# Performance work log

Hardware: AMD Instinct MI355X
Metric: run time of the kernel (lower is better)

The kernel has to match this reference:

```python
import jax, jax.numpy as jnp
import numpy as np

N, E, D, H = 100000, 800000, 128, 4
DK = D // H
SCALE = 1.0 / np.sqrt(D)  # keep logits tame with random weights
EPS = 1e-5


def _layernorm(x, g, b):
    mu = jnp.mean(x, axis=-1, keepdims=True)
    var = jnp.mean(jnp.square(x - mu), axis=-1, keepdims=True)
    return (x - mu) * jax.lax.rsqrt(var + EPS) * g + b


def setup_inputs() -> dict:
    key = jax.random.key(0)
    ks = jax.random.split(key, 14)
    inp = {
        'h': jax.random.normal(ks[0], (N, D), jnp.float32),
        'e_ij': jax.random.normal(ks[1], (E, D), jnp.float32),
        'W1': jax.random.normal(ks[2], (D, D), jnp.float32) * SCALE,
        'W2': jax.random.normal(ks[3], (D, D), jnp.float32) * SCALE,
        'W3': jax.random.normal(ks[4], (D, D), jnp.float32) * SCALE,
        'W4': jax.random.normal(ks[5], (D, D), jnp.float32) * SCALE,
        'W5': jax.random.normal(ks[6], (D, D), jnp.float32) * SCALE,
        'W6': jax.random.normal(ks[7], (D, D), jnp.float32) * SCALE,
        'ln_gamma': jnp.ones((D,), jnp.float32),
        'ln_beta': jnp.zeros((D,), jnp.float32),
        'mlp_w1': jax.random.normal(ks[8], (D, 2 * D), jnp.float32) * SCALE,
        'mlp_w2': jax.random.normal(ks[9], (2 * D, D), jnp.float32) * (1.0 / np.sqrt(2 * D)),
        'src': jax.random.randint(ks[10], (E,), 0, N, jnp.int32),
        'dst': jax.random.randint(ks[11], (E,), 0, N, jnp.int32),
    }
    return inp


def reference(h, e_ij, W1, W2, W3, W4, W5, W6, ln_gamma, ln_beta, mlp_w1, mlp_w2, src, dst):
    u = (h @ W1).reshape(N, H, DK)      # src-side query
    v = (h @ W2).reshape(N, H, DK)      # dst-side
    x3 = (e_ij @ W3).reshape(E, H, DK)
    # m = v[dst] + x_ij ; attn = u[src] * m (elementwise per head/channel)
    m = v[dst] + x3                      # [E,H,DK]
    attn = (u[src] * m) / np.sqrt(DK)    # [E,H,DK]
    # edge_softmax: segment softmax over incoming edges of each dst node
    amax = jax.ops.segment_max(attn, dst, num_segments=N)   # [N,H,DK]
    ex = jnp.exp(attn - amax[dst])
    denom = jax.ops.segment_sum(ex, dst, num_segments=N)    # [N,H,DK]
    alpha = ex / denom[dst]
    k = (h @ W4).reshape(N, H, DK)
    x5 = (e_ij @ W5).reshape(E, H, DK)
    m2 = k[dst] + x5                     # [E,H,DK]
    agg = jax.ops.segment_sum(alpha * m2, dst, num_segments=N).reshape(N, D)
    h1 = h @ W6 + agg
    h1 = _layernorm(h1, ln_gamma, ln_beta)
    mlp_out = jax.nn.relu(h1 @ mlp_w1) @ mlp_w2
    h2 = _layernorm(h1 + mlp_out, ln_gamma, ln_beta)  # same LayerNorm params reused
    return h2
```

## Files before the change

### kernel.cpp

```cpp
#include <hip/hip_runtime.h>
#include <hip/hip_bf16.h>

#define N_NODES 100000
#define N_EDGES 800000

typedef __attribute__((ext_vector_type(8))) short short8v;
typedef __attribute__((ext_vector_type(4))) float f32x4;

__device__ __forceinline__ unsigned short f2bf(float f) {
    __hip_bfloat16 b = __float2bfloat16(f);
    return *(unsigned short*)&b;
}
__device__ __forceinline__ float bf2f(unsigned short u) {
    return __uint_as_float((unsigned)u << 16);
}
__device__ __forceinline__ unsigned pack2(float lo, float hi) {
    return (unsigned)f2bf(lo) | ((unsigned)f2bf(hi) << 16);
}

__device__ __forceinline__ void gload_lds16(const void* g, void* l) {
    __builtin_amdgcn_global_load_lds(
        (const __attribute__((address_space(1))) unsigned int*)g,
        (__attribute__((address_space(3))) unsigned int*)l,
        16, 0, 0);
}

__device__ __forceinline__ int xcd_swizzle(int orig, int q, int r) {
    int xcd = orig & 7, loc = orig >> 3;
    return (xcd < r ? xcd * (q + 1) : r * (q + 1) + (xcd - r) * q) + loc;
}

__global__ __launch_bounds__(256) void hist_dst(
    const int* __restrict__ dst, int* __restrict__ counts)
{
    int e = blockIdx.x * 256 + threadIdx.x;
    if (e < N_EDGES) atomicAdd(&counts[dst[e]], 1);
}

__global__ __launch_bounds__(256) void scan_p1(
    const int* __restrict__ in, int* __restrict__ partials, int n)
{
    __shared__ int ws[4];
    int t = threadIdx.x, lane = t & 63, wv = t >> 6;
    int base = blockIdx.x * 1024;
    int s = 0;
#pragma unroll
    for (int i = 0; i < 4; ++i) {
        int idx = base + i * 256 + t;
        s += (idx < n) ? in[idx] : 0;
    }
#pragma unroll
    for (int off = 1; off < 64; off <<= 1) s += __shfl_xor(s, off);
    if (lane == 0) ws[wv] = s;
    __syncthreads();
    if (t == 0) partials[blockIdx.x] = ws[0] + ws[1] + ws[2] + ws[3];
}

__global__ __launch_bounds__(64) void scan_p2(
    int* __restrict__ partials, int nb, int* __restrict__ total_out)
{
    int lane = threadIdx.x;
    int carry = 0;
    for (int base = 0; base < nb; base += 64) {
        int idx = base + lane;
        int v = (idx < nb) ? partials[idx] : 0;
        int s = v;
#pragma unroll
        for (int off = 1; off < 64; off <<= 1) {
            int w = __shfl_up(s, off);
            if (lane >= off) s += w;
        }
        if (idx < nb) partials[idx] = s - v + carry;
        carry += __shfl(s, 63);
    }
    if (lane == 0) *total_out = carry;
}

__global__ __launch_bounds__(256) void scan_p3(
    const int* __restrict__ in, int* __restrict__ out, int* __restrict__ cursor,
    const int* __restrict__ partials, int n)
{
    __shared__ int ws[4];
    __shared__ int wpre[4];
    __shared__ int s_tot;
    int t = threadIdx.x, lane = t & 63, wv = t >> 6;
    int base = blockIdx.x * 1024;
    int carry = partials[blockIdx.x];
    for (int sub = 0; sub < 4; ++sub) {
        int idx = base + sub * 256 + t;
        int v = (idx < n) ? in[idx] : 0;
        int s = v;
#pragma unroll
        for (int off = 1; off < 64; off <<= 1) {
            int w = __shfl_up(s, off);
            if (lane >= off) s += w;
        }
        if (lane == 63) ws[wv] = s;
        __syncthreads();
        if (t == 0) {
            int a = 0;
#pragma unroll
            for (int i = 0; i < 4; ++i) { wpre[i] = a; a += ws[i]; }
            s_tot = a;
        }
        __syncthreads();
        int excl = s - v + wpre[wv] + carry;
        if (idx < n) { out[idx] = excl; if (cursor) cursor[idx] = excl; }
        carry += s_tot;
        __syncthreads();
    }
}

__global__ __launch_bounds__(256) void scatter_edges(
    const int* __restrict__ dst, const int* __restrict__ src,
    int* __restrict__ cursor,
    int* __restrict__ edge_ord, int* __restrict__ src_ord,
    int* __restrict__ dst_ord)
{
    int e = blockIdx.x * 256 + threadIdx.x;
    if (e < N_EDGES) {
        int d = dst[e];
        int pos = atomicAdd(&cursor[d], 1);
        edge_ord[pos] = e;
        src_ord[pos] = src[e];
        dst_ord[pos] = d;
    }
}

__global__ __launch_bounds__(256) void calc_npieces(
    const int* __restrict__ offsets, int* __restrict__ npieces)
{
    int n = blockIdx.x * 256 + threadIdx.x;
    if (n < N_NODES) {
        int b = offsets[n], e = offsets[n + 1];
        npieces[n] = (e > b) ? (((e - 1) >> 6) - (b >> 6) + 1) : 0;
    }
}

__global__ __launch_bounds__(256) void prep_weights(
    const float* __restrict__ W1, const float* __restrict__ W2,
    const float* __restrict__ W3, const float* __restrict__ W4,
    const float* __restrict__ W5, const float* __restrict__ W6,
    const float* __restrict__ mw1, const float* __restrict__ mw2,
    unsigned short* __restrict__ w3t, unsigned short* __restrict__ w5t,
    unsigned short* __restrict__ wcatt,
    unsigned short* __restrict__ mw1t, unsigned short* __restrict__ mw2t)
{
    int bid = blockIdx.x;
    if (bid < 64) {
        int t = bid * 256 + threadIdx.x;
        int r = t >> 7, c = t & 127;
        w3t[c * 128 + r] = f2bf(W3[t]);
        w5t[c * 128 + r] = f2bf(W5[t]);
    } else if (bid < 320) {
        int t = (bid - 64) * 256 + threadIdx.x;
        int n = t >> 7, k = t & 127;
        const float* Wm = (n < 128) ? W1 : (n < 256) ? W2 : (n < 384) ? W4 : W6;
        wcatt[t] = f2bf(Wm[k * 128 + (n & 127)]);
    } else {
        int t = (bid - 320) * 256 + threadIdx.x;
        if (t < 32768) {
            int n = t >> 7, k = t & 127;
            mw1t[t] = f2bf(mw1[k * 256 + n]);
        } else {
            int s = t - 32768;
            int n = s >> 8, k = s & 255;
            mw2t[s] = f2bf(mw2[k * 128 + n]);
        }
    }
}

__global__ __launch_bounds__(256) void gemm_node(
    const float* __restrict__ A, const unsigned short* __restrict__ Bt,
    unsigned short* __restrict__ uvkb, float* __restrict__ hw6f)
{
    const int nwg = 1563 * 4;
    const int l = xcd_swizzle((int)blockIdx.x, nwg >> 3, nwg & 7);
    const int m0 = (l >> 2) * 64;
    const int n0 = (l & 3) * 128;

    const int t = threadIdx.x;
    const int lane = t & 63, wv = t >> 6;
    const int l15 = lane & 15, kg = lane >> 4;
    const int M = N_NODES, K = 128;

    int arow = m0 + wv * 16 + l15;
    int arow_c = arow < M ? arow : M - 1;
    const float* ap = A + (size_t)arow_c * K + kg * 8;

    f32x4 acc[8];
#pragma unroll
    for (int nt = 0; nt < 8; ++nt) acc[nt] = (f32x4){0.f, 0.f, 0.f, 0.f};

    for (int ko = 0; ko < K; ko += 32) {
        float4 f0 = *(const float4*)(ap + ko);
        float4 f1 = *(const float4*)(ap + ko + 4);
        short8v af;
        af[0] = (short)f2bf(f0.x); af[1] = (short)f2bf(f0.y);
        af[2] = (short)f2bf(f0.z); af[3] = (short)f2bf(f0.w);
        af[4] = (short)f2bf(f1.x); af[5] = (short)f2bf(f1.y);
        af[6] = (short)f2bf(f1.z); af[7] = (short)f2bf(f1.w);
#pragma unroll
        for (int nt = 0; nt < 8; ++nt) {
            short8v bf = *(const short8v*)(Bt + (size_t)(n0 + nt * 16 + l15) * K + ko + kg * 8);
            acc[nt] = __builtin_amdgcn_mfma_f32_16x16x32_bf16(af, bf, acc[nt], 0, 0, 0);
        }
    }
#pragma unroll
    for (int nt = 0; nt < 8; ++nt) {
#pragma unroll
        for (int r = 0; r < 4; ++r) {
            int row = m0 + wv * 16 + kg * 4 + r;
            if (row < M) {
                int col = n0 + nt * 16 + l15;
                float vfl = acc[nt][r];
                if (n0 < 384) uvkb[(size_t)row * 384 + col] = f2bf(vfl);
                else          hw6f[(size_t)row * 128 + col - 384] = vfl;
            }
        }
    }
}

__global__ __launch_bounds__(256) void gemm_bf16(
    const unsigned short* __restrict__ A, const unsigned short* __restrict__ Bt,
    int M, int K, int Nc,
    const float* __restrict__ res, float* __restrict__ Cf,
    unsigned short* __restrict__ Cb, int do_relu)
{
    const int t = threadIdx.x;
    const int lane = t & 63, wv = t >> 6;
    const int l15 = lane & 15, kg = lane >> 4;
    const int m0 = blockIdx.x * 64;
    const int n0 = blockIdx.y * 128;

    int arow = m0 + wv * 16 + l15;
    int arow_c = arow < M ? arow : M - 1;
    const unsigned short* ap = A + (size_t)arow_c * K + kg * 8;

    f32x4 acc[8];
#pragma unroll
    for (int nt = 0; nt < 8; ++nt) acc[nt] = (f32x4){0.f, 0.f, 0.f, 0.f};

    for (int ko = 0; ko < K; ko += 32) {
        short8v af = *(const short8v*)(ap + ko);
#pragma unroll
        for (int nt = 0; nt < 8; ++nt) {
            short8v bf = *(const short8v*)(Bt + (size_t)(n0 + nt * 16 + l15) * K + ko + kg * 8);
            acc[nt] = __builtin_amdgcn_mfma_f32_16x16x32_bf16(af, bf, acc[nt], 0, 0, 0);
        }
    }
#pragma unroll
    for (int nt = 0; nt < 8; ++nt) {
#pragma unroll
        for (int r = 0; r < 4; ++r) {
            int row = m0 + wv * 16 + kg * 4 + r;
            if (row < M) {
                int col = n0 + nt * 16 + l15;
                float vfl = acc[nt][r];
                if (res) vfl += res[(size_t)row * Nc + col];
                if (do_relu) vfl = fmaxf(vfl, 0.f);
                if (Cf) Cf[(size_t)row * Nc + col] = vfl;
                else    Cb[(size_t)row * Nc + col] = f2bf(vfl);
            }
        }
    }
}

__global__ __launch_bounds__(256) void gemm_bf16_ln(
    const unsigned short* __restrict__ A, const unsigned short* __restrict__ Bt,
    int M, int K, const float* __restrict__ res,
    const float* __restrict__ gamma, const float* __restrict__ beta,
    float* __restrict__ out)
{
    const int t = threadIdx.x;
    const int lane = t & 63, wv = t >> 6;
    const int l15 = lane & 15, kg = lane >> 4;
    const int m0 = blockIdx.x * 64;

    int arow = m0 + wv * 16 + l15;
    int arow_c = arow < M ? arow : M - 1;
    const unsigned short* ap = A + (size_t)arow_c * K + kg * 8;

    f32x4 acc[8];
#pragma unroll
    for (int nt = 0; nt < 8; ++nt) acc[nt] = (f32x4){0.f, 0.f, 0.f, 0.f};

    for (int ko = 0; ko < K; ko += 32) {
        short8v af = *(const short8v*)(ap + ko);
#pragma unroll
        for (int nt = 0; nt < 8; ++nt) {
            short8v bf = *(const short8v*)(Bt + (size_t)(nt * 16 + l15) * K + ko + kg * 8);
            acc[nt] = __builtin_amdgcn_mfma_f32_16x16x32_bf16(af, bf, acc[nt], 0, 0, 0);
        }
    }

    float gv[8], bv[8];
#pragma unroll
    for (int nt = 0; nt < 8; ++nt) {
        gv[nt] = gamma[nt * 16 + l15];
        bv[nt] = beta[nt * 16 + l15];
    }

#pragma unroll
    for (int r = 0; r < 4; ++r) {
        int row = m0 + wv * 16 + kg * 4 + r;
        int rc = row < M ? row : M - 1;
        float x[8];
        float s = 0.f;
#pragma unroll
        for (int nt = 0; nt < 8; ++nt) {
            x[nt] = acc[nt][r] + res[(size_t)rc * 128 + nt * 16 + l15];
            s += x[nt];
        }
#pragma unroll
        for (int off = 1; off < 16; off <<= 1) s += __shfl_xor(s, off);
        float mu = s * (1.f / 128.f);
        float ss = 0.f;
#pragma unroll
        for (int nt = 0; nt < 8; ++nt) {
            float d = x[nt] - mu;
            ss += d * d;
        }
#pragma unroll
        for (int off = 1; off < 16; off <<= 1) ss += __shfl_xor(ss, off);
        float rsv = rsqrtf(ss * (1.f / 128.f) + 1e-5f);
        if (row < M) {
#pragma unroll
            for (int nt = 0; nt < 8; ++nt)
                out[(size_t)row * 128 + nt * 16 + l15] =
                    (x[nt] - mu) * rsv * gv[nt] + bv[nt];
        }
    }
}

__global__ __launch_bounds__(256, 4) void edge_agg(
    const float* __restrict__ e_ij,
    const unsigned short* __restrict__ w3t, const unsigned short* __restrict__ w5t,
    const unsigned short* __restrict__ uvkb,
    const int* __restrict__ edge_ord, const int* __restrict__ src_ord,
    const int* __restrict__ dst_ord,
    const int* __restrict__ offsets, const int* __restrict__ ppos,
    float* __restrict__ dpart, float* __restrict__ apart)
{
    __shared__ __align__(16) float e_s[64 * 128];
    __shared__ int s_eid[64], s_src[64], s_dst[64];
    __shared__ int s_sb[64], s_se[64], s_pi[64];
    __shared__ int s_nseg;

    const int t  = threadIdx.x;
    const int lane = t & 63, wv = t >> 6;
    const int l15 = lane & 15, kg = lane >> 4;
    const int cb = wv * 32 + 2 * l15;
    const float inv = 0.17677669529663687f;

    const int nwg = N_EDGES / 64;
    const int bswz = xcd_swizzle((int)blockIdx.x, nwg >> 3, nwg & 7);
    const int e0 = bswz * 64;

    if (t < 64) {
        s_eid[t] = edge_ord[e0 + t];
        s_src[t] = src_ord[e0 + t];
        int d = dst_ord[e0 + t];
        s_dst[t] = d;
        int dprev = __shfl_up(d, 1);
        bool bnd = (t == 0) || (d != dprev);
        unsigned long long mask = __ballot(bnd);
        int sid = __popcll(mask & ((1ull << t) - 1ull));
        if (bnd) {
            s_sb[sid] = t;
            s_pi[sid] = ppos[d] + bswz - (offsets[d] >> 6);
            if (t > 0) s_se[sid - 1] = t;
        }
        if (t == 63) {
            int ns = __popcll(mask);
            s_se[ns - 1] = 64;
            s_nseg = ns;
        }
    }
    __syncthreads();

#pragma unroll
    for (int i = 0; i < 8; ++i) {
        int c = i * 256 + t;
        int row = c >> 5, j = c & 31;
        int js = j ^ (row & 7);
        const float* g = e_ij + (size_t)s_eid[row] * 128 + js * 4;
        void* l = (void*)((char*)(&e_s[0]) + (size_t)i * 4096 + (size_t)wv * 1024);
        gload_lds16(g, l);
    }
    __syncthreads();

    unsigned short* eb = (unsigned short*)&e_s[0];
    {
        const int crow = t >> 2, q = t & 3;
        float4 fr[8];
#pragma unroll
        for (int i = 0; i < 8; ++i) {
            int j = (q * 8 + i) ^ (crow & 7);
            fr[i] = *(const float4*)(&e_s[crow * 128 + j * 4]);
        }
        __syncthreads();
#pragma unroll
        for (int i = 0; i < 4; ++i) {
            short8v pk;
            pk[0] = (short)f2bf(fr[2 * i].x);     pk[1] = (short)f2bf(fr[2 * i].y);
            pk[2] = (short)f2bf(fr[2 * i].z);     pk[3] = (short)f2bf(fr[2 * i].w);
            pk[4] = (short)f2bf(fr[2 * i + 1].x); pk[5] = (short)f2bf(fr[2 * i + 1].y);
            pk[6] = (short)f2bf(fr[2 * i + 1].z); pk[7] = (short)f2bf(fr[2 * i + 1].w);
            int c = (q * 4 + i) ^ (crow & 15);
            *(short8v*)(eb + crow * 128 + c * 8) = pk;
        }
    }
    __syncthreads();

    const int nseg = __builtin_amdgcn_readfirstlane(s_nseg);

    f32x4 a3[4][2], a5[4][2];
#pragma unroll
    for (int m = 0; m < 4; ++m) {
        a3[m][0] = (f32x4){0.f, 0.f, 0.f, 0.f};
        a3[m][1] = (f32x4){0.f, 0.f, 0.f, 0.f};
        a5[m][0] = (f32x4){0.f, 0.f, 0.f, 0.f};
        a5[m][1] = (f32x4){0.f, 0.f, 0.f, 0.f};
    }
    {
        const unsigned short* b3p0 = w3t + (size_t)(cb + 0) * 128 + kg * 8;
        const unsigned short* b3p1 = w3t + (size_t)(cb + 1) * 128 + kg * 8;
        const unsigned short* b5p0 = w5t + (size_t)(cb + 0) * 128 + kg * 8;
        const unsigned short* b5p1 = w5t + (size_t)(cb + 1) * 128 + kg * 8;
#pragma unroll
        for (int kidx = 0; kidx < 4; ++kidx) {
            const int ko = kidx * 32;
            short8v b30 = *(const short8v*)(b3p0 + ko);
            short8v b31 = *(const short8v*)(b3p1 + ko);
            short8v b50 = *(const short8v*)(b5p0 + ko);
            short8v b51 = *(const short8v*)(b5p1 + ko);
#pragma unroll
            for (int m = 0; m < 4; ++m) {
                const int row = m * 16 + l15;
                short8v af = *(const short8v*)(eb + row * 128 + (((kidx << 2) | kg) ^ l15) * 8);
                a3[m][0] = __builtin_amdgcn_mfma_f32_16x16x32_bf16(af, b30, a3[m][0], 0, 0, 0);
                a3[m][1] = __builtin_amdgcn_mfma_f32_16x16x32_bf16(af, b31, a3[m][1], 0, 0, 0);
                a5[m][0] = __builtin_amdgcn_mfma_f32_16x16x32_bf16(af, b50, a5[m][0], 0, 0, 0);
                a5[m][1] = __builtin_amdgcn_mfma_f32_16x16x32_bf16(af, b51, a5[m][1], 0, 0, 0);
            }
        }
    }

#pragma unroll
    for (int m = 0; m < 4; ++m) {
#pragma unroll
        for (int r = 0; r < 4; ++r) {
            int le = m * 16 + kg * 4 + r;
            int d  = s_dst[le];
            int sv = s_src[le];
            unsigned upk = *(const unsigned*)&uvkb[(size_t)sv * 384 + cb];
            unsigned vpk = *(const unsigned*)&uvkb[(size_t)d * 384 + 128 + cb];
            float u0 = bf2f((unsigned short)(upk & 0xffffu));
            float u1 = bf2f((unsigned short)(upk >> 16));
            float v0 = bf2f((unsigned short)(vpk & 0xffffu));
            float v1 = bf2f((unsigned short)(vpk >> 16));
            float at0 = u0 * (v0 + a3[m][0][r]) * inv;
            float at1 = u1 * (v1 + a3[m][1][r]) * inv;
            float ex0 = __expf(fminf(at0, 80.f));
            float ex1 = __expf(fminf(at1, 80.f));
            a3[m][0][r] = ex0;
            a3[m][1][r] = ex1;
            a5[m][0][r] = ex0 * a5[m][0][r];
            a5[m][1][r] = ex1 * a5[m][1][r];
        }
    }

    for (int sg = 0; sg < nseg; ++sg) {
        const int b  = __builtin_amdgcn_readfirstlane(s_sb[sg]);
        const int e2 = __builtin_amdgcn_readfirstlane(s_se[sg]);
        const int pi = __builtin_amdgcn_readfirstlane(s_pi[sg]);
        float d0 = 0.f, d1 = 0.f, g0 = 0.f, g1 = 0.f;
#pragma unroll
        for (int m = 0; m < 4; ++m) {
            if (b < m * 16 + 16 && e2 > m * 16) {
#pragma unroll
                for (int r = 0; r < 4; ++r) {
                    int slot = m * 16 + kg * 4 + r;
                    bool in = (slot >= b) && (slot < e2);
                    d0 += in ? a3[m][0][r] : 0.f;
                    d1 += in ? a3[m][1][r] : 0.f;
                    g0 += in ? a5[m][0][r] : 0.f;
                    g1 += in ? a5[m][1][r] : 0.f;
                }
            }
        }
        d0 += __shfl_xor(d0, 16); d0 += __shfl_xor(d0, 32);
        d1 += __shfl_xor(d1, 16); d1 += __shfl_xor(d1, 32);
        g0 += __shfl_xor(g0, 16); g0 += __shfl_xor(g0, 32);
        g1 += __shfl_xor(g1, 16); g1 += __shfl_xor(g1, 32);
        if (kg == 0) {
            *(float2*)&dpart[(size_t)pi * 128 + cb] = make_float2(d0, d1);
            *(float2*)&apart[(size_t)pi * 128 + cb] = make_float2(g0, g1);
        }
    }
}

__global__ __launch_bounds__(256) void node_finalize(
    const float* __restrict__ hw6f, const unsigned short* __restrict__ uvkb,
    const float* __restrict__ dpart, const float* __restrict__ apart,
    const int* __restrict__ ppos,
    const float* __restrict__ gamma, const float* __restrict__ beta,
    float* __restrict__ h1, unsigned short* __restrict__ h1b)
{
    int n = blockIdx.x * 4 + (threadIdx.x >> 6);
    int lane = threadIdx.x & 63;
    int p0 = ppos[n], p1 = ppos[n + 1];
    float de0 = 0.f, de1 = 0.f, g0 = 0.f, g1 = 0.f;
    for (int j = p0; j < p1; ++j) {
        float2 dv = *(const float2*)&dpart[(size_t)j * 128 + lane * 2];
        float2 av = *(const float2*)&apart[(size_t)j * 128 + lane * 2];
        de0 += dv.x; de1 += dv.y;
        g0  += av.x; g1  += av.y;
    }
    unsigned kpk = *(const unsigned*)&uvkb[(size_t)n * 384 + 256 + lane * 2];
    float k0 = bf2f((unsigned short)(kpk & 0xffffu));
    float k1 = bf2f((unsigned short)(kpk >> 16));
    float2 hw = *(const float2*)&hw6f[(size_t)n * 128 + lane * 2];
    float x0 = hw.x + (de0 > 0.f ? k0 + g0 / de0 : 0.f);
    float x1 = hw.y + (de1 > 0.f ? k1 + g1 / de1 : 0.f);
    float s = x0 + x1;
#pragma unroll
    for (int off = 1; off < 64; off <<= 1) s += __shfl_xor(s, off);
    float mu = s * (1.f / 128.f);
    float d0 = x0 - mu, d1 = x1 - mu;
    float ss = d0 * d0 + d1 * d1;
#pragma unroll
    for (int off = 1; off < 64; off <<= 1) ss += __shfl_xor(ss, off);
    float rs = rsqrtf(ss * (1.f / 128.f) + 1e-5f);
    float2 g = *(const float2*)&gamma[lane * 2];
    float2 b = *(const float2*)&beta[lane * 2];
    float o0 = d0 * rs * g.x + b.x;
    float o1 = d1 * rs * g.y + b.y;
    size_t base = (size_t)n * 128 + lane * 2;
    *(float2*)&h1[base] = make_float2(o0, o1);
    *(unsigned*)&h1b[base] = pack2(o0, o1);
}

extern "C" void kernel_launch(void* const* d_in, const int* in_sizes, int n_in,
                              void* d_out, int out_size, void* d_ws, size_t ws_size,
                              hipStream_t stream)
{
    const float* h    = (const float*)d_in[0];
    const float* e_ij = (const float*)d_in[1];
    const float* W1   = (const float*)d_in[2];
    const float* W2   = (const float*)d_in[3];
    const float* W3   = (const float*)d_in[4];
    const float* W4   = (const float*)d_in[5];
    const float* W5   = (const float*)d_in[6];
    const float* W6   = (const float*)d_in[7];
    const float* ln_g = (const float*)d_in[8];
    const float* ln_b = (const float*)d_in[9];
    const float* mw1  = (const float*)d_in[10];
    const float* mw2  = (const float*)d_in[11];
    const int*   src  = (const int*)d_in[12];
    const int*   dst  = (const int*)d_in[13];
    float* out = (float*)d_out;

    float* ws = (float*)d_ws;
    float* hw6f  = ws;
    float* h1    = ws + 12800000;
    float* dpart = ws + 25600000;
    float* apart = ws + 40100000;
    unsigned short* uvkb    = (unsigned short*)(ws + 54600000);
    unsigned short* h1b     = (unsigned short*)(ws + 73800000);
    unsigned short* hiddenb = (unsigned short*)(ws + 80200000);
    unsigned short* w3t   = (unsigned short*)(ws + 93000000);
    unsigned short* w5t   = w3t + 16384;
    unsigned short* wcatt = w5t + 16384;
    unsigned short* mw1t  = wcatt + 65536;
    unsigned short* mw2t  = mw1t + 32768;
    int* ibase    = (int*)(ws + 93100000);
    int* counts   = ibase;
    int* offsets  = ibase + 100000;
    int* cursor   = ibase + 200001;
    int* npieces  = ibase + 300001;
    int* ppos     = ibase + 400001;
    int* partials = ibase + 500102;
    int* edge_ord = ibase + 500230;
    int* src_ord  = edge_ord + N_EDGES;
    int* dst_ord  = src_ord + N_EDGES;

    dim3 blk(256);
    hipMemsetAsync(counts, 0, N_NODES * sizeof(int), stream);

    hist_dst<<<N_EDGES / 256, blk, 0, stream>>>(dst, counts);
    scan_p1<<<98, blk, 0, stream>>>(counts, partials, N_NODES);
    scan_p2<<<1, 64, 0, stream>>>(partials, 98, offsets + N_NODES);
    scan_p3<<<98, blk, 0, stream>>>(counts, offsets, cursor, partials, N_NODES);
    scatter_edges<<<N_EDGES / 256, blk, 0, stream>>>(dst, src, cursor,
                                                     edge_ord, src_ord, dst_ord);
    calc_npieces<<<391, blk, 0, stream>>>(offsets, npieces);
    scan_p1<<<98, blk, 0, stream>>>(npieces, partials, N_NODES);
    scan_p2<<<1, 64, 0, stream>>>(partials, 98, ppos + N_NODES);
    scan_p3<<<98, blk, 0, stream>>>(npieces, ppos, (int*)nullptr, partials, N_NODES);

    prep_weights<<<576, blk, 0, stream>>>(W1, W2, W3, W4, W5, W6, mw1, mw2,
                                          w3t, w5t, wcatt, mw1t, mw2t);

    gemm_node<<<1563 * 4, blk, 0, stream>>>(h, wcatt, uvkb, hw6f);

    edge_agg<<<N_EDGES / 64, blk, 0, stream>>>(e_ij, w3t, w5t, uvkb,
                                               edge_ord, src_ord, dst_ord,
                                               offsets, ppos, dpart, apart);

    node_finalize<<<N_NODES / 4, blk, 0, stream>>>(hw6f, uvkb, dpart, apart, ppos,
                                                   ln_g, ln_b, h1, h1b);

    gemm_bf16<<<dim3(1563, 2), blk, 0, stream>>>(h1b, mw1t, N_NODES, 128, 256,
                                                 nullptr, nullptr, hiddenb, 1);
    gemm_bf16_ln<<<1563, blk, 0, stream>>>(hiddenb, mw2t, N_NODES, 256,
                                           h1, ln_g, ln_b, out);
}
```

Baseline: 636.9 us.

## Fuse node finalize, MLP GEMMs and final LayerNorm into one kernel

```diff
diff --git a/kernel.cpp b/kernel.cpp
--- a/kernel.cpp
+++ b/kernel.cpp
@@ -174,14 +174,11 @@
     const float* __restrict__ A, const unsigned short* __restrict__ Bt,
     unsigned short* __restrict__ uvkb, float* __restrict__ hw6f)
 {
-    const int nwg = 1563 * 4;
-    const int l = xcd_swizzle((int)blockIdx.x, nwg >> 3, nwg & 7);
-    const int m0 = (l >> 2) * 64;
-    const int n0 = (l & 3) * 128;
-
     const int t = threadIdx.x;
     const int lane = t & 63, wv = t >> 6;
     const int l15 = lane & 15, kg = lane >> 4;
+    const int m0 = blockIdx.x * 64;
+    const int n0 = blockIdx.y * 128;
     const int M = N_NODES, K = 128;
 
     int arow = m0 + wv * 16 + l15;
@@ -217,118 +214,6 @@
                 if (n0 < 384) uvkb[(size_t)row * 384 + col] = f2bf(vfl);
                 else          hw6f[(size_t)row * 128 + col - 384] = vfl;
             }
-        }
-    }
-}
-
-__global__ __launch_bounds__(256) void gemm_bf16(
-    const unsigned short* __restrict__ A, const unsigned short* __restrict__ Bt,
-    int M, int K, int Nc,
-    const float* __restrict__ res, float* __restrict__ Cf,
-    unsigned short* __restrict__ Cb, int do_relu)
-{
-    const int t = threadIdx.x;
-    const int lane = t & 63, wv = t >> 6;
-    const int l15 = lane & 15, kg = lane >> 4;
-    const int m0 = blockIdx.x * 64;
-    const int n0 = blockIdx.y * 128;
-
-    int arow = m0 + wv * 16 + l15;
-    int arow_c = arow < M ? arow : M - 1;
-    const unsigned short* ap = A + (size_t)arow_c * K + kg * 8;
-
-    f32x4 acc[8];
-#pragma unroll
-    for (int nt = 0; nt < 8; ++nt) acc[nt] = (f32x4){0.f, 0.f, 0.f, 0.f};
-
-    for (int ko = 0; ko < K; ko += 32) {
-        short8v af = *(const short8v*)(ap + ko);
-#pragma unroll
-        for (int nt = 0; nt < 8; ++nt) {
-            short8v bf = *(const short8v*)(Bt + (size_t)(n0 + nt * 16 + l15) * K + ko + kg * 8);
-            acc[nt] = __builtin_amdgcn_mfma_f32_16x16x32_bf16(af, bf, acc[nt], 0, 0, 0);
-        }
-    }
-#pragma unroll
-    for (int nt = 0; nt < 8; ++nt) {
-#pragma unroll
-        for (int r = 0; r < 4; ++r) {
-            int row = m0 + wv * 16 + kg * 4 + r;
-            if (row < M) {
-                int col = n0 + nt * 16 + l15;
-                float vfl = acc[nt][r];
-                if (res) vfl += res[(size_t)row * Nc + col];
-                if (do_relu) vfl = fmaxf(vfl, 0.f);
-                if (Cf) Cf[(size_t)row * Nc + col] = vfl;
-                else    Cb[(size_t)row * Nc + col] = f2bf(vfl);
-            }
-        }
-    }
-}
-
-__global__ __launch_bounds__(256) void gemm_bf16_ln(
-    const unsigned short* __restrict__ A, const unsigned short* __restrict__ Bt,
-    int M, int K, const float* __restrict__ res,
-    const float* __restrict__ gamma, const float* __restrict__ beta,
-    float* __restrict__ out)
-{
-    const int t = threadIdx.x;
-    const int lane = t & 63, wv = t >> 6;
-    const int l15 = lane & 15, kg = lane >> 4;
-    const int m0 = blockIdx.x * 64;
-
-    int arow = m0 + wv * 16 + l15;
-    int arow_c = arow < M ? arow : M - 1;
-    const unsigned short* ap = A + (size_t)arow_c * K + kg * 8;
-
-    f32x4 acc[8];
-#pragma unroll
-    for (int nt = 0; nt < 8; ++nt) acc[nt] = (f32x4){0.f, 0.f, 0.f, 0.f};
-
-    for (int ko = 0; ko < K; ko += 32) {
-        short8v af = *(const short8v*)(ap + ko);
-#pragma unroll
-        for (int nt = 0; nt < 8; ++nt) {
-            short8v bf = *(const short8v*)(Bt + (size_t)(nt * 16 + l15) * K + ko + kg * 8);
-            acc[nt] = __builtin_amdgcn_mfma_f32_16x16x32_bf16(af, bf, acc[nt], 0, 0, 0);
-        }
-    }
-
-    float gv[8], bv[8];
-#pragma unroll
-    for (int nt = 0; nt < 8; ++nt) {
-        gv[nt] = gamma[nt * 16 + l15];
-        bv[nt] = beta[nt * 16 + l15];
-    }
-
-#pragma unroll
-    for (int r = 0; r < 4; ++r) {
-        int row = m0 + wv * 16 + kg * 4 + r;
-        int rc = row < M ? row : M - 1;
-        float x[8];
-        float s = 0.f;
-#pragma unroll
-        for (int nt = 0; nt < 8; ++nt) {
-            x[nt] = acc[nt][r] + res[(size_t)rc * 128 + nt * 16 + l15];
-            s += x[nt];
-        }
-#pragma unroll
-        for (int off = 1; off < 16; off <<= 1) s += __shfl_xor(s, off);
-        float mu = s * (1.f / 128.f);
-        float ss = 0.f;
-#pragma unroll
-        for (int nt = 0; nt < 8; ++nt) {
-            float d = x[nt] - mu;
-            ss += d * d;
-        }
-#pragma unroll
-        for (int off = 1; off < 16; off <<= 1) ss += __shfl_xor(ss, off);
-        float rsv = rsqrtf(ss * (1.f / 128.f) + 1e-5f);
-        if (row < M) {
-#pragma unroll
-            for (int nt = 0; nt < 8; ++nt)
-                out[(size_t)row * 128 + nt * 16 + l15] =
-                    (x[nt] - mu) * rsv * gv[nt] + bv[nt];
         }
     }
 }
@@ -501,45 +386,142 @@
     }
 }
 
-__global__ __launch_bounds__(256) void node_finalize(
+__global__ __launch_bounds__(256, 2) void node_tail(
     const float* __restrict__ hw6f, const unsigned short* __restrict__ uvkb,
     const float* __restrict__ dpart, const float* __restrict__ apart,
     const int* __restrict__ ppos,
+    const unsigned short* __restrict__ mw1t, const unsigned short* __restrict__ mw2t,
     const float* __restrict__ gamma, const float* __restrict__ beta,
-    float* __restrict__ h1, unsigned short* __restrict__ h1b)
-{
-    int n = blockIdx.x * 4 + (threadIdx.x >> 6);
-    int lane = threadIdx.x & 63;
-    int p0 = ppos[n], p1 = ppos[n + 1];
-    float de0 = 0.f, de1 = 0.f, g0 = 0.f, g1 = 0.f;
-    for (int j = p0; j < p1; ++j) {
-        float2 dv = *(const float2*)&dpart[(size_t)j * 128 + lane * 2];
-        float2 av = *(const float2*)&apart[(size_t)j * 128 + lane * 2];
-        de0 += dv.x; de1 += dv.y;
-        g0  += av.x; g1  += av.y;
-    }
-    unsigned kpk = *(const unsigned*)&uvkb[(size_t)n * 384 + 256 + lane * 2];
-    float k0 = bf2f((unsigned short)(kpk & 0xffffu));
-    float k1 = bf2f((unsigned short)(kpk >> 16));
-    float2 hw = *(const float2*)&hw6f[(size_t)n * 128 + lane * 2];
-    float x0 = hw.x + (de0 > 0.f ? k0 + g0 / de0 : 0.f);
-    float x1 = hw.y + (de1 > 0.f ? k1 + g1 / de1 : 0.f);
-    float s = x0 + x1;
-#pragma unroll
-    for (int off = 1; off < 64; off <<= 1) s += __shfl_xor(s, off);
-    float mu = s * (1.f / 128.f);
-    float d0 = x0 - mu, d1 = x1 - mu;
-    float ss = d0 * d0 + d1 * d1;
-#pragma unroll
-    for (int off = 1; off < 64; off <<= 1) ss += __shfl_xor(ss, off);
-    float rs = rsqrtf(ss * (1.f / 128.f) + 1e-5f);
-    float2 g = *(const float2*)&gamma[lane * 2];
-    float2 b = *(const float2*)&beta[lane * 2];
-    float o0 = d0 * rs * g.x + b.x;
-    float o1 = d1 * rs * g.y + b.y;
-    size_t base = (size_t)n * 128 + lane * 2;
-    *(float2*)&h1[base] = make_float2(o0, o1);
-    *(unsigned*)&h1b[base] = pack2(o0, o1);
+    float* __restrict__ out)
+{
+    __shared__ __align__(16) float h1f[64 * 132];
+    __shared__ __align__(16) unsigned short hid[64 * 264];
+
+    const int t = threadIdx.x;
+    const int lane = t & 63, wv = t >> 6;
+    const int l15 = lane & 15, kg = lane >> 4;
+    const int nb = blockIdx.x * 64;
+
+    for (int i = 0; i < 16; ++i) {
+        int row = wv * 16 + i;
+        int n = nb + row;
+        int nc = n < N_NODES ? n : N_NODES - 1;
+        int p0 = ppos[nc], p1 = ppos[nc + 1];
+        float de0 = 0.f, de1 = 0.f, g0 = 0.f, g1 = 0.f;
+        for (int j = p0; j < p1; ++j) {
+            float2 dv = *(const float2*)&dpart[(size_t)j * 128 + lane * 2];
+            float2 av = *(const float2*)&apart[(size_t)j * 128 + lane * 2];
+            de0 += dv.x; de1 += dv.y;
+            g0  += av.x; g1  += av.y;
+        }
+        unsigned kpk = *(const unsigned*)&uvkb[(size_t)nc * 384 + 256 + lane * 2];
+        float k0 = bf2f((unsigned short)(kpk & 0xffffu));
+        float k1 = bf2f((unsigned short)(kpk >> 16));
+        float2 hw = *(const float2*)&hw6f[(size_t)nc * 128 + lane * 2];
+        float x0 = hw.x + (de0 > 0.f ? k0 + g0 / de0 : 0.f);
+        float x1 = hw.y + (de1 > 0.f ? k1 + g1 / de1 : 0.f);
+        float s = x0 + x1;
+#pragma unroll
+        for (int off = 1; off < 64; off <<= 1) s += __shfl_xor(s, off);
+        float mu = s * (1.f / 128.f);
+        float d0 = x0 - mu, d1 = x1 - mu;
+        float ss = d0 * d0 + d1 * d1;
+#pragma unroll
+        for (int off = 1; off < 64; off <<= 1) ss += __shfl_xor(ss, off);
+        float rs = rsqrtf(ss * (1.f / 128.f) + 1e-5f);
+        float2 g = *(const float2*)&gamma[lane * 2];
+        float2 b = *(const float2*)&beta[lane * 2];
+        h1f[row * 132 + lane * 2]     = d0 * rs * g.x + b.x;
+        h1f[row * 132 + lane * 2 + 1] = d1 * rs * g.y + b.y;
+    }
+    __syncthreads();
+
+    {
+        const int arow = wv * 16 + l15;
+        f32x4 acc[16];
+#pragma unroll
+        for (int nt = 0; nt < 16; ++nt) acc[nt] = (f32x4){0.f, 0.f, 0.f, 0.f};
+#pragma unroll
+        for (int kidx = 0; kidx < 4; ++kidx) {
+            const int ko = kidx * 32;
+            const float* rp = &h1f[arow * 132 + ko + kg * 8];
+            float4 f0 = *(const float4*)rp;
+            float4 f1 = *(const float4*)(rp + 4);
+            short8v af;
+            af[0] = (short)f2bf(f0.x); af[1] = (short)f2bf(f0.y);
+            af[2] = (short)f2bf(f0.z); af[3] = (short)f2bf(f0.w);
+            af[4] = (short)f2bf(f1.x); af[5] = (short)f2bf(f1.y);
+            af[6] = (short)f2bf(f1.z); af[7] = (short)f2bf(f1.w);
+#pragma unroll
+            for (int nt = 0; nt < 16; ++nt) {
+                short8v bf = *(const short8v*)(mw1t + (size_t)(nt * 16 + l15) * 128 + ko + kg * 8);
+                acc[nt] = __builtin_amdgcn_mfma_f32_16x16x32_bf16(af, bf, acc[nt], 0, 0, 0);
+            }
+        }
+#pragma unroll
+        for (int nt = 0; nt < 16; ++nt) {
+#pragma unroll
+            for (int r = 0; r < 4; ++r) {
+                int row = wv * 16 + kg * 4 + r;
+                int col = nt * 16 + l15;
+                hid[row * 264 + col] = f2bf(fmaxf(acc[nt][r], 0.f));
+            }
+        }
+    }
+    __syncthreads();
+
+    {
+        const int arow = wv * 16 + l15;
+        f32x4 acc[8];
+#pragma unroll
+        for (int nt = 0; nt < 8; ++nt) acc[nt] = (f32x4){0.f, 0.f, 0.f, 0.f};
+#pragma unroll
+        for (int kidx = 0; kidx < 8; ++kidx) {
+            const int ko = kidx * 32;
+            short8v af = *(const short8v*)&hid[arow * 264 + ko + kg * 8];
+#pragma unroll
+            for (int nt = 0; nt < 8; ++nt) {
+                short8v bf = *(const short8v*)(mw2t + (size_t)(nt * 16 + l15) * 256 + ko + kg * 8);
+                acc[nt] = __builtin_amdgcn_mfma_f32_16x16x32_bf16(af, bf, acc[nt], 0, 0, 0);
+            }
+        }
+        float gv[8], bv[8];
+#pragma unroll
+        for (int nt = 0; nt < 8; ++nt) {
+            gv[nt] = gamma[nt * 16 + l15];
+            bv[nt] = beta[nt * 16 + l15];
+        }
+#pragma unroll
+        for (int r = 0; r < 4; ++r) {
+            int lrow = wv * 16 + kg * 4 + r;
+            int grow = nb + lrow;
+            float x[8];
+            float s = 0.f;
+#pragma unroll
+            for (int nt = 0; nt < 8; ++nt) {
+                x[nt] = acc[nt][r] + h1f[lrow * 132 + nt * 16 + l15];
+                s += x[nt];
+            }
+#pragma unroll
+            for (int off = 1; off < 16; off <<= 1) s += __shfl_xor(s, off);
+            float mu = s * (1.f / 128.f);
+            float ss = 0.f;
+#pragma unroll
+            for (int nt = 0; nt < 8; ++nt) {
+                float d = x[nt] - mu;
+                ss += d * d;
+            }
+#pragma unroll
+            for (int off = 1; off < 16; off <<= 1) ss += __shfl_xor(ss, off);
+            float rsv = rsqrtf(ss * (1.f / 128.f) + 1e-5f);
+            if (grow < N_NODES) {
+#pragma unroll
+                for (int nt = 0; nt < 8; ++nt)
+                    out[(size_t)grow * 128 + nt * 16 + l15] =
+                        (x[nt] - mu) * rsv * gv[nt] + bv[nt];
+            }
+        }
+    }
 }
 
 extern "C" void kernel_launch(void* const* d_in, const int* in_sizes, int n_in,
@@ -564,12 +546,9 @@
 
     float* ws = (float*)d_ws;
     float* hw6f  = ws;
-    float* h1    = ws + 12800000;
     float* dpart = ws + 25600000;
     float* apart = ws + 40100000;
-    unsigned short* uvkb    = (unsigned short*)(ws + 54600000);
-    unsigned short* h1b     = (unsigned short*)(ws + 73800000);
-    unsigned short* hiddenb = (unsigned short*)(ws + 80200000);
+    unsigned short* uvkb  = (unsigned short*)(ws + 54600000);
     unsigned short* w3t   = (unsigned short*)(ws + 93000000);
     unsigned short* w5t   = w3t + 16384;
     unsigned short* wcatt = w5t + 16384;
@@ -603,17 +582,12 @@
     prep_weights<<<576, blk, 0, stream>>>(W1, W2, W3, W4, W5, W6, mw1, mw2,
                                           w3t, w5t, wcatt, mw1t, mw2t);
 
-    gemm_node<<<1563 * 4, blk, 0, stream>>>(h, wcatt, uvkb, hw6f);
+    gemm_node<<<dim3(1563, 4), blk, 0, stream>>>(h, wcatt, uvkb, hw6f);
 
     edge_agg<<<N_EDGES / 64, blk, 0, stream>>>(e_ij, w3t, w5t, uvkb,
                                                edge_ord, src_ord, dst_ord,
                                                offsets, ppos, dpart, apart);
 
-    node_finalize<<<N_NODES / 4, blk, 0, stream>>>(hw6f, uvkb, dpart, apart, ppos,
-                                                   ln_g, ln_b, h1, h1b);
-
-    gemm_bf16<<<dim3(1563, 2), blk, 0, stream>>>(h1b, mw1t, N_NODES, 128, 256,
-                                                 nullptr, nullptr, hiddenb, 1);
-    gemm_bf16_ln<<<1563, blk, 0, stream>>>(hiddenb, mw2t, N_NODES, 256,
-                                           h1, ln_g, ln_b, out);
-}
+    node_tail<<<1563, blk, 0, stream>>>(hw6f, uvkb, dpart, apart, ppos,
+                                        mw1t, mw2t, ln_g, ln_b, out);
+}
```

New measurement: 672.7 us. 5.6% more time.
